# Kernel optimization log

Measured on AMD Instinct MI355X. Metric: run time of the kernel, lower is better.

Reference implementation:

```python
import jax, jax.numpy as jnp
import numpy as np

EMB = 1024
HID = 1024
VOCAB = 50257


def _lstm_cell(x, h, c, Wih, Whh, bih, bhh):
    # PyTorch gate order: i, f, g, o
    gates = x @ Wih.T + bih + h @ Whh.T + bhh  # [1, 4H]
    i, f, g, o = jnp.split(gates, 4, axis=-1)
    c_new = jax.nn.sigmoid(f) * c + jax.nn.sigmoid(i) * jnp.tanh(g)
    h_new = jax.nn.sigmoid(o) * jnp.tanh(c_new)
    return h_new, c_new


def setup_inputs() -> dict:
    key = jax.random.key(0)
    ks = jax.random.split(key, 16)
    s = 0.02
    return {
        "word_input": jax.random.randint(ks[0], (1,), 0, VOCAB),
        "h0": jax.random.normal(ks[1], (2, 1, HID), jnp.float32),
        "c0": jax.random.normal(ks[2], (2, 1, HID), jnp.float32),
        "emb": jax.random.normal(ks[3], (VOCAB, EMB), jnp.float32) * s,
        "W_ih0": jax.random.normal(ks[4], (4 * HID, EMB), jnp.float32) * s,
        "W_hh0": jax.random.normal(ks[5], (4 * HID, HID), jnp.float32) * s,
        "b_ih0": jax.random.normal(ks[6], (4 * HID,), jnp.float32) * s,
        "b_hh0": jax.random.normal(ks[7], (4 * HID,), jnp.float32) * s,
        "W_ih1": jax.random.normal(ks[8], (4 * HID, HID), jnp.float32) * s,
        "W_hh1": jax.random.normal(ks[9], (4 * HID, HID), jnp.float32) * s,
        "b_ih1": jax.random.normal(ks[10], (4 * HID,), jnp.float32) * s,
        "b_hh1": jax.random.normal(ks[11], (4 * HID,), jnp.float32) * s,
        "W_out": jax.random.normal(ks[12], (VOCAB, HID), jnp.float32) * s,
        "b_out": jax.random.normal(ks[13], (VOCAB,), jnp.float32) * s,
    }


def reference(word_input, h0, c0, emb, W_ih0, W_hh0, b_ih0, b_hh0,
              W_ih1, W_hh1, b_ih1, b_hh1, W_out, b_out):
    # embedding lookup + ReLU, batch=1 seq=1
    x = jax.nn.relu(emb[word_input])                 # [1, EMB]
    # 2-layer LSTM single step (dropout disabled / eval mode)
    h1, c1 = _lstm_cell(x, h0[0], c0[0], W_ih0, W_hh0, b_ih0, b_hh0)
    h2, c2 = _lstm_cell(h1, h0[1], c0[1], W_ih1, W_hh1, b_ih1, b_hh1)
    logits = h2 @ W_out.T + b_out                    # [1, VOCAB]
    log_probas = jax.nn.log_softmax(logits, axis=1)
    h_out = jnp.stack([h1, h2])                      # [2, 1, HID]
    c_out = jnp.stack([c1, c2])
    return log_probas, (h_out, c_out)
```

## Files before the change

### kernel.cpp

```cpp
#include <hip/hip_runtime.h>
#include <math.h>

#define EMB 1024
#define HID 1024
#define VOCAB 50257
#define HOUT_OFF VOCAB
#define COUT_OFF (VOCAB + 2*HID)
#define RPB 16
#define NB_LOGITS ((VOCAB + RPB - 1) / RPB)

__device__ __forceinline__ float wave_reduce(float v) {
#pragma unroll
    for (int o = 32; o > 0; o >>= 1) v += __shfl_down(v, o);
    return v;
}

__device__ __forceinline__ float sigmoidf_(float x) { return 1.0f / (1.0f + expf(-x)); }

__global__ __launch_bounds__(256) void lstm_gemv(
    const float* __restrict__ Wih, const float* __restrict__ Whh,
    const float* __restrict__ bih, const float* __restrict__ bhh,
    const float* __restrict__ emb, const int* __restrict__ word,
    const float* __restrict__ x_in,
    const float* __restrict__ h_prev, const float* __restrict__ c_prev,
    float* __restrict__ h_ws, float* __restrict__ out, int layer)
{
    const int r    = blockIdx.x;
    const int wave = threadIdx.x >> 6;
    const int lane = threadIdx.x & 63;
    const int row  = wave * HID + r;

    float4 xv[4], hv[4];
    if (x_in != nullptr) {
#pragma unroll
        for (int j = 0; j < 4; ++j) xv[j] = ((const float4*)x_in)[j*64 + lane];
    } else {
        const float4* e = (const float4*)(emb + (size_t)word[0] * EMB);
#pragma unroll
        for (int j = 0; j < 4; ++j) {
            float4 v = e[j*64 + lane];
            v.x = fmaxf(v.x, 0.f); v.y = fmaxf(v.y, 0.f);
            v.z = fmaxf(v.z, 0.f); v.w = fmaxf(v.w, 0.f);
            xv[j] = v;
        }
    }
#pragma unroll
    for (int j = 0; j < 4; ++j) hv[j] = ((const float4*)h_prev)[j*64 + lane];

    const float4* wih = (const float4*)(Wih + (size_t)row * EMB);
    const float4* whh = (const float4*)(Whh + (size_t)row * HID);
    float acc = 0.f;
#pragma unroll
    for (int j = 0; j < 4; ++j) {
        float4 a = wih[j*64 + lane];
        acc += a.x*xv[j].x + a.y*xv[j].y + a.z*xv[j].z + a.w*xv[j].w;
        float4 b = whh[j*64 + lane];
        acc += b.x*hv[j].x + b.y*hv[j].y + b.z*hv[j].z + b.w*hv[j].w;
    }
    acc = wave_reduce(acc);

    __shared__ float gates[4];
    if (lane == 0) gates[wave] = acc + bih[row] + bhh[row];
    __syncthreads();

    if (threadIdx.x == 0) {
        float ig = sigmoidf_(gates[0]);
        float fg = sigmoidf_(gates[1]);
        float gg = tanhf(gates[2]);
        float og = sigmoidf_(gates[3]);
        float c  = fg * c_prev[r] + ig * gg;
        float h  = og * tanhf(c);
        h_ws[r] = h;
        out[HOUT_OFF + layer * HID + r] = h;
        out[COUT_OFF + layer * HID + r] = c;
    }
}

__global__ __launch_bounds__(256) void logits_gemv(
    const float* __restrict__ W, const float* __restrict__ b,
    const float* __restrict__ x, float* __restrict__ out,
    float* __restrict__ partials)
{
    const int tid = threadIdx.x;
    const int l   = tid & 15;
    const int row = blockIdx.x * RPB + (tid >> 4);

    __shared__ float lg[RPB];
    if (tid < RPB) lg[tid] = -INFINITY;
    __syncthreads();

    float a0 = 0.f, a1 = 0.f, a2 = 0.f, a3 = 0.f;
    if (row < VOCAB) {
        const float4* __restrict__ wr = (const float4*)(W + (size_t)row * HID);
        const float4* __restrict__ xp = (const float4*)x;
#pragma unroll
        for (int j = 0; j < 4; ++j) {
            float4 w0 = wr[l + 16*(4*j+0)], x0 = xp[l + 16*(4*j+0)];
            float4 w1 = wr[l + 16*(4*j+1)], x1 = xp[l + 16*(4*j+1)];
            float4 w2 = wr[l + 16*(4*j+2)], x2 = xp[l + 16*(4*j+2)];
            float4 w3 = wr[l + 16*(4*j+3)], x3 = xp[l + 16*(4*j+3)];
            a0 += w0.x*x0.x + w0.y*x0.y + w0.z*x0.z + w0.w*x0.w;
            a1 += w1.x*x1.x + w1.y*x1.y + w1.z*x1.z + w1.w*x1.w;
            a2 += w2.x*x2.x + w2.y*x2.y + w2.z*x2.z + w2.w*x2.w;
            a3 += w3.x*x3.x + w3.y*x3.y + w3.z*x3.z + w3.w*x3.w;
        }
    }
    float acc = (a0 + a1) + (a2 + a3);
    acc += __shfl_xor(acc, 8);
    acc += __shfl_xor(acc, 4);
    acc += __shfl_xor(acc, 2);
    acc += __shfl_xor(acc, 1);

    if (l == 0 && row < VOCAB) {
        float logit = acc + b[row];
        out[row] = logit;
        lg[tid >> 4] = logit;
    }
    __syncthreads();

    if (tid == 0) {
        float M = -INFINITY, S = 0.f;
#pragma unroll
        for (int i = 0; i < RPB; ++i) {
            float v = lg[i];
            if (v > -INFINITY) {
                float nm = fmaxf(M, v);
                S = S * expf(M - nm) + expf(v - nm);
                M = nm;
            }
        }
        partials[2 * blockIdx.x]     = M;
        partials[2 * blockIdx.x + 1] = S;
    }
}

__global__ __launch_bounds__(256) void logsoftmax_sub(
    float* __restrict__ out, const float* __restrict__ partials, int nb, int n)
{
    float M = -INFINITY, S = 0.f;
    for (int p = threadIdx.x; p < nb; p += 256) {
        float m = partials[2*p], s = partials[2*p + 1];
        float nm = fmaxf(M, m);
        S = S * expf(M - nm) + s * expf(m - nm);
        M = nm;
    }
    __shared__ float ms[256], ss[256];
    ms[threadIdx.x] = M; ss[threadIdx.x] = S;
    __syncthreads();
    for (int o = 128; o > 0; o >>= 1) {
        if (threadIdx.x < (unsigned)o) {
            float m2 = ms[threadIdx.x + o], s2 = ss[threadIdx.x + o];
            float m1 = ms[threadIdx.x];
            float nm = fmaxf(m1, m2);
            ss[threadIdx.x] = ss[threadIdx.x] * expf(m1 - nm) + s2 * expf(m2 - nm);
            ms[threadIdx.x] = nm;
        }
        __syncthreads();
    }
    float Z = ms[0] + logf(ss[0]);
    int i = blockIdx.x * 256 + threadIdx.x;
    if (i < n) out[i] -= Z;
}

extern "C" void kernel_launch(void* const* d_in, const int* in_sizes, int n_in,
                              void* d_out, int out_size, void* d_ws, size_t ws_size,
                              hipStream_t stream)
{
    const int*   word = (const int*)  d_in[0];
    const float* h0   = (const float*)d_in[1];
    const float* c0   = (const float*)d_in[2];
    const float* emb  = (const float*)d_in[3];
    const float* Wih0 = (const float*)d_in[4];
    const float* Whh0 = (const float*)d_in[5];
    const float* bih0 = (const float*)d_in[6];
    const float* bhh0 = (const float*)d_in[7];
    const float* Wih1 = (const float*)d_in[8];
    const float* Whh1 = (const float*)d_in[9];
    const float* bih1 = (const float*)d_in[10];
    const float* bhh1 = (const float*)d_in[11];
    const float* Wout = (const float*)d_in[12];
    const float* bout = (const float*)d_in[13];

    float* out = (float*)d_out;
    float* ws  = (float*)d_ws;
    float* h1       = ws;
    float* h2       = ws + HID;
    float* partials = ws + 2 * HID;

    lstm_gemv<<<HID, 256, 0, stream>>>(Wih0, Whh0, bih0, bhh0, emb, word,
                                       nullptr, h0, c0, h1, out, 0);
    lstm_gemv<<<HID, 256, 0, stream>>>(Wih1, Whh1, bih1, bhh1, emb, word,
                                       h1, h0 + HID, c0 + HID, h2, out, 1);
    logits_gemv<<<NB_LOGITS, 256, 0, stream>>>(Wout, bout, h2, out, partials);
    logsoftmax_sub<<<(VOCAB + 255) / 256, 256, 0, stream>>>(out, partials,
                                                            NB_LOGITS, VOCAB);
}
```

Baseline: 438.3 us.

## Fuse LSTM layers, logits GEMV and log-softmax into one persistent kernel with grid barriers

```diff
diff --git a/kernel.cpp b/kernel.cpp
--- a/kernel.cpp
+++ b/kernel.cpp
@@ -4,10 +4,16 @@
 #define EMB 1024
 #define HID 1024
 #define VOCAB 50257
+#define NBLK 512
+#define RPB 99
+#define NBLK_LG ((VOCAB + RPB - 1) / RPB)
 #define HOUT_OFF VOCAB
 #define COUT_OFF (VOCAB + 2*HID)
-#define RPB 16
-#define NB_LOGITS ((VOCAB + RPB - 1) / RPB)
+
+#define H1_OFF 16
+#define H2_OFF (16 + HID)
+#define MP_OFF (16 + 2*HID)
+#define SP_OFF (MP_OFF + NBLK)
 
 __device__ __forceinline__ float wave_reduce(float v) {
 #pragma unroll
@@ -17,149 +23,190 @@
 
 __device__ __forceinline__ float sigmoidf_(float x) { return 1.0f / (1.0f + expf(-x)); }
 
-__global__ __launch_bounds__(256) void lstm_gemv(
+__global__ void init_bar(unsigned* __restrict__ bar) {
+    if (threadIdx.x < 3) bar[threadIdx.x] = 0u;
+}
+
+__device__ __forceinline__ void grid_barrier(unsigned* ctr) {
+    __syncthreads();
+    if (threadIdx.x == 0) {
+        __threadfence();
+        __hip_atomic_fetch_add(ctr, 1u, __ATOMIC_ACQ_REL, __HIP_MEMORY_SCOPE_AGENT);
+        while (__hip_atomic_load(ctr, __ATOMIC_ACQUIRE, __HIP_MEMORY_SCOPE_AGENT) < NBLK)
+            __builtin_amdgcn_s_sleep(1);
+    }
+    __syncthreads();
+}
+
+__device__ __forceinline__ void lstm_unit_step(
+    int unit, int wave, int lane,
+    const float4* __restrict__ xp, bool do_relu,
     const float* __restrict__ Wih, const float* __restrict__ Whh,
     const float* __restrict__ bih, const float* __restrict__ bhh,
-    const float* __restrict__ emb, const int* __restrict__ word,
-    const float* __restrict__ x_in,
-    const float* __restrict__ h_prev, const float* __restrict__ c_prev,
-    float* __restrict__ h_ws, float* __restrict__ out, int layer)
+    const float4* __restrict__ hp, const float* __restrict__ c_prev,
+    float* __restrict__ h_dst, float* __restrict__ out_h, float* __restrict__ out_c,
+    float* gates)
 {
-    const int r    = blockIdx.x;
-    const int wave = threadIdx.x >> 6;
-    const int lane = threadIdx.x & 63;
-    const int row  = wave * HID + r;
-
-    float4 xv[4], hv[4];
-    if (x_in != nullptr) {
-#pragma unroll
-        for (int j = 0; j < 4; ++j) xv[j] = ((const float4*)x_in)[j*64 + lane];
-    } else {
-        const float4* e = (const float4*)(emb + (size_t)word[0] * EMB);
-#pragma unroll
-        for (int j = 0; j < 4; ++j) {
-            float4 v = e[j*64 + lane];
-            v.x = fmaxf(v.x, 0.f); v.y = fmaxf(v.y, 0.f);
-            v.z = fmaxf(v.z, 0.f); v.w = fmaxf(v.w, 0.f);
-            xv[j] = v;
-        }
-    }
-#pragma unroll
-    for (int j = 0; j < 4; ++j) hv[j] = ((const float4*)h_prev)[j*64 + lane];
-
+    const int row = wave * HID + unit;
     const float4* wih = (const float4*)(Wih + (size_t)row * EMB);
     const float4* whh = (const float4*)(Whh + (size_t)row * HID);
     float acc = 0.f;
 #pragma unroll
     for (int j = 0; j < 4; ++j) {
+        float4 xv = xp[j*64 + lane];
+        if (do_relu) {
+            xv.x = fmaxf(xv.x, 0.f); xv.y = fmaxf(xv.y, 0.f);
+            xv.z = fmaxf(xv.z, 0.f); xv.w = fmaxf(xv.w, 0.f);
+        }
         float4 a = wih[j*64 + lane];
-        acc += a.x*xv[j].x + a.y*xv[j].y + a.z*xv[j].z + a.w*xv[j].w;
-        float4 b = whh[j*64 + lane];
-        acc += b.x*hv[j].x + b.y*hv[j].y + b.z*hv[j].z + b.w*hv[j].w;
+        acc += a.x*xv.x + a.y*xv.y + a.z*xv.z + a.w*xv.w;
+        float4 hv = hp[j*64 + lane];
+        float4 bw = whh[j*64 + lane];
+        acc += bw.x*hv.x + bw.y*hv.y + bw.z*hv.z + bw.w*hv.w;
     }
     acc = wave_reduce(acc);
-
-    __shared__ float gates[4];
     if (lane == 0) gates[wave] = acc + bih[row] + bhh[row];
     __syncthreads();
-
-    if (threadIdx.x == 0) {
+    if (wave == 0 && lane == 0) {
         float ig = sigmoidf_(gates[0]);
         float fg = sigmoidf_(gates[1]);
         float gg = tanhf(gates[2]);
         float og = sigmoidf_(gates[3]);
-        float c  = fg * c_prev[r] + ig * gg;
+        float c  = fg * c_prev[unit] + ig * gg;
         float h  = og * tanhf(c);
-        h_ws[r] = h;
-        out[HOUT_OFF + layer * HID + r] = h;
-        out[COUT_OFF + layer * HID + r] = c;
-    }
-}
-
-__global__ __launch_bounds__(256) void logits_gemv(
-    const float* __restrict__ W, const float* __restrict__ b,
-    const float* __restrict__ x, float* __restrict__ out,
-    float* __restrict__ partials)
+        h_dst[unit] = h;
+        out_h[unit] = h;
+        out_c[unit] = c;
+    }
+    __syncthreads();
+}
+
+__global__ __launch_bounds__(256) void fused_decoder(
+    const float* __restrict__ emb, const int* __restrict__ word,
+    const float* __restrict__ Wih0, const float* __restrict__ Whh0,
+    const float* __restrict__ bih0, const float* __restrict__ bhh0,
+    const float* __restrict__ Wih1, const float* __restrict__ Whh1,
+    const float* __restrict__ bih1, const float* __restrict__ bhh1,
+    const float* __restrict__ Wout, const float* __restrict__ bout,
+    const float* __restrict__ h0, const float* __restrict__ c0,
+    float* __restrict__ out, float* __restrict__ ws)
 {
-    const int tid = threadIdx.x;
-    const int l   = tid & 15;
-    const int row = blockIdx.x * RPB + (tid >> 4);
-
-    __shared__ float lg[RPB];
-    if (tid < RPB) lg[tid] = -INFINITY;
-    __syncthreads();
-
-    float a0 = 0.f, a1 = 0.f, a2 = 0.f, a3 = 0.f;
-    if (row < VOCAB) {
-        const float4* __restrict__ wr = (const float4*)(W + (size_t)row * HID);
-        const float4* __restrict__ xp = (const float4*)x;
-#pragma unroll
-        for (int j = 0; j < 4; ++j) {
-            float4 w0 = wr[l + 16*(4*j+0)], x0 = xp[l + 16*(4*j+0)];
-            float4 w1 = wr[l + 16*(4*j+1)], x1 = xp[l + 16*(4*j+1)];
-            float4 w2 = wr[l + 16*(4*j+2)], x2 = xp[l + 16*(4*j+2)];
-            float4 w3 = wr[l + 16*(4*j+3)], x3 = xp[l + 16*(4*j+3)];
-            a0 += w0.x*x0.x + w0.y*x0.y + w0.z*x0.z + w0.w*x0.w;
-            a1 += w1.x*x1.x + w1.y*x1.y + w1.z*x1.z + w1.w*x1.w;
-            a2 += w2.x*x2.x + w2.y*x2.y + w2.z*x2.z + w2.w*x2.w;
-            a3 += w3.x*x3.x + w3.y*x3.y + w3.z*x3.z + w3.w*x3.w;
-        }
-    }
-    float acc = (a0 + a1) + (a2 + a3);
-    acc += __shfl_xor(acc, 8);
-    acc += __shfl_xor(acc, 4);
-    acc += __shfl_xor(acc, 2);
-    acc += __shfl_xor(acc, 1);
-
-    if (l == 0 && row < VOCAB) {
-        float logit = acc + b[row];
-        out[row] = logit;
-        lg[tid >> 4] = logit;
-    }
-    __syncthreads();
-
-    if (tid == 0) {
+    const int b = blockIdx.x, tid = threadIdx.x;
+    const int wave = tid >> 6, lane = tid & 63;
+    unsigned* bar = (unsigned*)ws;
+    float* h1 = ws + H1_OFF;
+    float* h2 = ws + H2_OFF;
+    float* mp = ws + MP_OFF;
+    float* sp = ws + SP_OFF;
+
+    __shared__ float gates[4];
+    __shared__ float ms16[16], ss16[16];
+    __shared__ float red_m[256], red_s[256];
+
+    {
+        const float4* xp = (const float4*)(emb + (size_t)word[0] * EMB);
+        const float4* hp = (const float4*)h0;
+        lstm_unit_step(2*b+0, wave, lane, xp, true, Wih0, Whh0, bih0, bhh0,
+                       hp, c0, h1, out + HOUT_OFF, out + COUT_OFF, gates);
+        lstm_unit_step(2*b+1, wave, lane, xp, true, Wih0, Whh0, bih0, bhh0,
+                       hp, c0, h1, out + HOUT_OFF, out + COUT_OFF, gates);
+    }
+    grid_barrier(&bar[0]);
+
+    {
+        const float4* xp = (const float4*)h1;
+        const float4* hp = (const float4*)(h0 + HID);
+        lstm_unit_step(2*b+0, wave, lane, xp, false, Wih1, Whh1, bih1, bhh1,
+                       hp, c0 + HID, h2, out + HOUT_OFF + HID, out + COUT_OFF + HID, gates);
+        lstm_unit_step(2*b+1, wave, lane, xp, false, Wih1, Whh1, bih1, bhh1,
+                       hp, c0 + HID, h2, out + HOUT_OFF + HID, out + COUT_OFF + HID, gates);
+    }
+    grid_barrier(&bar[1]);
+
+    {
+        const int l = tid & 15, g = tid >> 4;
+        const int base = b * RPB;
+        const int rend = (base + RPB < VOCAB) ? base + RPB : VOCAB;
         float M = -INFINITY, S = 0.f;
-#pragma unroll
-        for (int i = 0; i < RPB; ++i) {
-            float v = lg[i];
-            if (v > -INFINITY) {
-                float nm = fmaxf(M, v);
-                S = S * expf(M - nm) + expf(v - nm);
+        const float4* xp = (const float4*)h2;
+        if (b < NBLK_LG) {
+            for (int it = 0; it < 7; ++it) {
+                const int row = base + it*16 + g;
+                if (row < rend) {
+                    const float4* wr = (const float4*)(Wout + (size_t)row * HID);
+                    float a0 = 0.f, a1 = 0.f, a2 = 0.f, a3 = 0.f;
+#pragma unroll
+                    for (int j = 0; j < 4; ++j) {
+                        float4 w0 = wr[l+16*(4*j+0)], x0 = xp[l+16*(4*j+0)];
+                        float4 w1 = wr[l+16*(4*j+1)], x1 = xp[l+16*(4*j+1)];
+                        float4 w2 = wr[l+16*(4*j+2)], x2 = xp[l+16*(4*j+2)];
+                        float4 w3 = wr[l+16*(4*j+3)], x3 = xp[l+16*(4*j+3)];
+                        a0 += w0.x*x0.x + w0.y*x0.y + w0.z*x0.z + w0.w*x0.w;
+                        a1 += w1.x*x1.x + w1.y*x1.y + w1.z*x1.z + w1.w*x1.w;
+                        a2 += w2.x*x2.x + w2.y*x2.y + w2.z*x2.z + w2.w*x2.w;
+                        a3 += w3.x*x3.x + w3.y*x3.y + w3.z*x3.z + w3.w*x3.w;
+                    }
+                    float acc = (a0 + a1) + (a2 + a3);
+                    acc += __shfl_xor(acc, 8);
+                    acc += __shfl_xor(acc, 4);
+                    acc += __shfl_xor(acc, 2);
+                    acc += __shfl_xor(acc, 1);
+                    if (l == 0) {
+                        float logit = acc + bout[row];
+                        out[row] = logit;
+                        float nm = fmaxf(M, logit);
+                        S = S * expf(M - nm) + expf(logit - nm);
+                        M = nm;
+                    }
+                }
+            }
+        }
+        if (l == 0) { ms16[g] = M; ss16[g] = S; }
+        __syncthreads();
+        if (tid == 0 && b < NBLK_LG) {
+            float Mb = -INFINITY, Sb = 0.f;
+#pragma unroll
+            for (int i2 = 0; i2 < 16; ++i2) {
+                float m = ms16[i2];
+                if (m > -INFINITY) {
+                    float nm = fmaxf(Mb, m);
+                    Sb = Sb * expf(Mb - nm) + ss16[i2] * expf(m - nm);
+                    Mb = nm;
+                }
+            }
+            mp[b] = Mb; sp[b] = Sb;
+        }
+    }
+    grid_barrier(&bar[2]);
+
+    {
+        float M = -INFINITY, S = 0.f;
+        for (int p = tid; p < NBLK_LG; p += 256) {
+            float m = mp[p];
+            if (m > -INFINITY) {
+                float s = sp[p];
+                float nm = fmaxf(M, m);
+                S = S * expf(M - nm) + s * expf(m - nm);
                 M = nm;
             }
         }
-        partials[2 * blockIdx.x]     = M;
-        partials[2 * blockIdx.x + 1] = S;
-    }
-}
-
-__global__ __launch_bounds__(256) void logsoftmax_sub(
-    float* __restrict__ out, const float* __restrict__ partials, int nb, int n)
-{
-    float M = -INFINITY, S = 0.f;
-    for (int p = threadIdx.x; p < nb; p += 256) {
-        float m = partials[2*p], s = partials[2*p + 1];
-        float nm = fmaxf(M, m);
-        S = S * expf(M - nm) + s * expf(m - nm);
-        M = nm;
-    }
-    __shared__ float ms[256], ss[256];
-    ms[threadIdx.x] = M; ss[threadIdx.x] = S;
-    __syncthreads();
-    for (int o = 128; o > 0; o >>= 1) {
-        if (threadIdx.x < (unsigned)o) {
-            float m2 = ms[threadIdx.x + o], s2 = ss[threadIdx.x + o];
-            float m1 = ms[threadIdx.x];
-            float nm = fmaxf(m1, m2);
-            ss[threadIdx.x] = ss[threadIdx.x] * expf(m1 - nm) + s2 * expf(m2 - nm);
-            ms[threadIdx.x] = nm;
-        }
+        red_m[tid] = M; red_s[tid] = S;
         __syncthreads();
-    }
-    float Z = ms[0] + logf(ss[0]);
-    int i = blockIdx.x * 256 + threadIdx.x;
-    if (i < n) out[i] -= Z;
+        for (int o = 128; o > 0; o >>= 1) {
+            if (tid < o) {
+                float m1 = red_m[tid], s1 = red_s[tid];
+                float m2 = red_m[tid+o], s2 = red_s[tid+o];
+                float nm = fmaxf(m1, m2);
+                red_s[tid] = s1 * expf(m1 - nm) + s2 * expf(m2 - nm);
+                red_m[tid] = nm;
+            }
+            __syncthreads();
+        }
+        const float Z = red_m[0] + logf(red_s[0]);
+        const int base = b * RPB;
+        const int rend = (base + RPB < VOCAB) ? base + RPB : VOCAB;
+        for (int i = base + tid; i < rend; i += 256) out[i] -= Z;
+    }
 }
 
 extern "C" void kernel_launch(void* const* d_in, const int* in_sizes, int n_in,
@@ -183,15 +230,9 @@
 
     float* out = (float*)d_out;
     float* ws  = (float*)d_ws;
-    float* h1       = ws;
-    float* h2       = ws + HID;
-    float* partials = ws + 2 * HID;
-
-    lstm_gemv<<<HID, 256, 0, stream>>>(Wih0, Whh0, bih0, bhh0, emb, word,
-                                       nullptr, h0, c0, h1, out, 0);
-    lstm_gemv<<<HID, 256, 0, stream>>>(Wih1, Whh1, bih1, bhh1, emb, word,
-                                       h1, h0 + HID, c0 + HID, h2, out, 1);
-    logits_gemv<<<NB_LOGITS, 256, 0, stream>>>(Wout, bout, h2, out, partials);
-    logsoftmax_sub<<<(VOCAB + 255) / 256, 256, 0, stream>>>(out, partials,
-                                                            NB_LOGITS, VOCAB);
-}
+
+    init_bar<<<1, 64, 0, stream>>>((unsigned*)ws);
+    fused_decoder<<<NBLK, 256, 0, stream>>>(emb, word, Wih0, Whh0, bih0, bhh0,
+                                            Wih1, Whh1, bih1, bhh1, Wout, bout,
+                                            h0, c0, out, ws);
+}
```

Result: slower. 548.2 us (+25.1%).
